# Optimization experiments

Hardware: AMD Instinct MI355X
Metric: run time of the kernel (lower is better)

The kernel has to match this reference:

```python
import jax, jax.numpy as jnp
import numpy as np

N_USER = 50000
N_ITEM = 50000
DIM = 128
HID = DIM // 2
E = 500000
SLOPE = 0.2  # GATv2 negative_slope default


def _glorot(key, shape):
    fan_in = shape[0]
    return jax.random.normal(key, shape, dtype=jnp.float32) / np.sqrt(fan_in)


def setup_inputs() -> dict:
    key = jax.random.key(0)
    ks = jax.random.split(key, 32)
    inp = {
        "x_user": jax.random.normal(ks[0], (N_USER, DIM), dtype=jnp.float32),
        "x_item": jax.random.normal(ks[1], (N_ITEM, DIM), dtype=jnp.float32),
        # edge[0] = source indices, edge[1] = destination indices
        "edge_u2i": jnp.stack([
            jax.random.randint(ks[2], (E,), 0, N_USER),
            jax.random.randint(ks[3], (E,), 0, N_ITEM),
        ]),
        "edge_i2u": jnp.stack([
            jax.random.randint(ks[4], (E,), 0, N_ITEM),
            jax.random.randint(ks[5], (E,), 0, N_USER),
        ]),
    }
    # per-node-type projection MLP: Linear(dim, dim//2) -> ReLU -> Linear(dim//2, dim)
    i = 6
    for t in ("user", "item"):
        inp[f"W1_{t}"] = _glorot(ks[i], (DIM, HID)); i += 1
        inp[f"b1_{t}"] = jnp.zeros((HID,), jnp.float32)
        inp[f"W2_{t}"] = _glorot(ks[i], (HID, DIM)); i += 1
        inp[f"b2_{t}"] = jnp.zeros((DIM,), jnp.float32)
    # per-edge-type GATv2 params (heads=1): lin_l (src), lin_r (dst), att, out bias
    for r in ("u2i", "i2u"):
        inp[f"Wl_{r}"] = _glorot(ks[i], (DIM, DIM)); i += 1
        inp[f"bl_{r}"] = jnp.zeros((DIM,), jnp.float32)
        inp[f"Wr_{r}"] = _glorot(ks[i], (DIM, DIM)); i += 1
        inp[f"br_{r}"] = jnp.zeros((DIM,), jnp.float32)
        inp[f"att_{r}"] = _glorot(ks[i], (DIM,)); i += 1
        inp[f"bias_{r}"] = jnp.zeros((DIM,), jnp.float32)
    return inp


def _mlp(x, W1, b1, W2, b2):
    return jax.nn.relu(x @ W1 + b1) @ W2 + b2


def _gatv2(x_src, x_dst, edge, Wl, bl, Wr, br, att, bias, n_dst):
    src, dst = edge[0], edge[1]
    xl = x_src @ Wl + bl                                    # [Ns, D]
    xr = x_dst @ Wr + br                                    # [Nd, D]
    z = jax.nn.leaky_relu(xl[src] + xr[dst], SLOPE)         # [E, D] gather
    logit = z @ att                                          # [E]
    # per-destination softmax over incoming edges
    m = jax.ops.segment_max(logit, dst, num_segments=n_dst)
    e = jnp.exp(logit - m[dst])
    s = jax.ops.segment_sum(e, dst, num_segments=n_dst)
    alpha = e / (s[dst] + 1e-16)                             # [E]
    out = jax.ops.segment_sum(alpha[:, None] * xl[src], dst, num_segments=n_dst)
    return out + bias


def reference(x_user, x_item, edge_u2i, edge_i2u,
              W1_user, b1_user, W2_user, b2_user,
              W1_item, b1_item, W2_item, b2_item,
              Wl_u2i, bl_u2i, Wr_u2i, br_u2i, att_u2i, bias_u2i,
              Wl_i2u, bl_i2u, Wr_i2u, br_i2u, att_i2u, bias_i2u):
    hu = _mlp(x_user, W1_user, b1_user, W2_user, b2_user)
    hi = _mlp(x_item, W1_item, b1_item, W2_item, b2_item)
    # HeteroConv with aggr='sum'; each dst type receives from one relation here
    out_item = _gatv2(hu, hi, edge_u2i, Wl_u2i, bl_u2i, Wr_u2i, br_u2i, att_u2i, bias_u2i, N_ITEM)
    out_user = _gatv2(hi, hu, edge_i2u, Wl_i2u, bl_i2u, Wr_i2u, br_i2u, att_i2u, bias_i2u, N_USER)
    return jnp.stack([out_user, out_item])  # [2, N, D] (N_USER == N_ITEM)
```

## Files before the change

kernel.cpp:

```cpp
#include <hip/hip_runtime.h>
#include <hip/hip_bf16.h>
#include <math.h>

#define N_NODES 50000
#define DIM 128
#define HID 64
#define SLOPE 0.2f
#define CAP 64
#define TRASH (2 * N_NODES * CAP)

typedef __attribute__((ext_vector_type(8))) short bf16x8;
typedef __attribute__((ext_vector_type(4))) float f32x4;
typedef __fp16 h2 __attribute__((ext_vector_type(2)));

#define OW1 0
#define OW2 8192
#define OWL 16384
#define OWR 32768
#define BLOB 49152
#define PREPB 192

static __device__ __forceinline__ ushort f2bf(float f) {
    uint u = __float_as_uint(f);
    u += 0x7FFFu + ((u >> 16) & 1u);
    return (ushort)(u >> 16);
}

static __device__ __forceinline__ uint pkh(float a, float b) {
    h2 r = __builtin_amdgcn_cvt_pkrtz(a, b);
    return __builtin_bit_cast(uint, r);
}

static __device__ __forceinline__ void prep_one(
    const float* __restrict__ W1, const float* __restrict__ W2,
    const float* __restrict__ Wl, const float* __restrict__ Wr,
    ushort* __restrict__ blob, int idx)
{
    const float* W; int NN, nkt, rel;
    if (idx < OW2)      { W = W1; NN = 64;  nkt = 4; rel = idx; }
    else if (idx < OWL) { W = W2; NN = 128; nkt = 2; rel = idx - OW2; }
    else if (idx < OWR) { W = Wl; NN = 128; nkt = 4; rel = idx - OWL; }
    else                { W = Wr; NN = 128; nkt = 4; rel = idx - OWR; }
    int j = rel & 7, l = (rel >> 3) & 63, t = rel >> 9;
    int kt = t % nkt, n = t / nkt;
    int k   = kt * 32 + (l >> 4) * 8 + j;
    int col = n * 16 + (l & 15);
    blob[idx] = f2bf(W[k * NN + col]);
}

__global__ __launch_bounds__(256) void prep_weights(
    const float* __restrict__ W1u, const float* __restrict__ W2u,
    const float* __restrict__ Wlu, const float* __restrict__ Wru,
    ushort* __restrict__ blobU,
    const float* __restrict__ W1i, const float* __restrict__ W2i,
    const float* __restrict__ Wli, const float* __restrict__ Wri,
    ushort* __restrict__ blobI,
    int* __restrict__ counts2)
{
    const int bid = blockIdx.x;
    const int gtid = bid * 256 + threadIdx.x;
    if (gtid < 2 * N_NODES) counts2[gtid] = 0;
    if (bid < PREPB) {
        prep_one(W1u, W2u, Wlu, Wru, blobU, bid * 256 + threadIdx.x);
    } else if (bid < 2 * PREPB) {
        prep_one(W1i, W2i, Wli, Wri, blobI, (bid - PREPB) * 256 + threadIdx.x);
    }
}

__global__ __launch_bounds__(512, 4) void k2_node_fill(
    const float* __restrict__ xA, const ushort* __restrict__ blobA,
    const float* __restrict__ b1A, const float* __restrict__ b2A,
    const float* __restrict__ blA, const float* __restrict__ brA,
    ushort* __restrict__ XLA, ushort* __restrict__ XRA,
    const float* __restrict__ xB, const ushort* __restrict__ blobB,
    const float* __restrict__ b1B, const float* __restrict__ b2B,
    const float* __restrict__ blB, const float* __restrict__ brB,
    ushort* __restrict__ XLB, ushort* __restrict__ XRB,
    int gnt, int M,
    const int* __restrict__ e1, int E1, const int* __restrict__ e2, int E2,
    int* __restrict__ counts2, ushort* __restrict__ slots16, int fillCount)
{
    __shared__ ushort hstage_all[8 * 16 * 136];
    const int tid = threadIdx.x;

    int bid = blockIdx.x;
    const int four = fillCount * 4;
    int wid; bool isfill;
    if (bid < four) {
        if ((bid & 3) == 3) { isfill = true;  wid = bid >> 2; }
        else                { isfill = false; wid = (bid >> 2) * 3 + (bid & 3); }
    } else { isfill = false; wid = 3 * fillCount + (bid - four); }

    if (isfill) {
        const int t = wid * 512 + tid;
        const int n1 = (E1 + 15) >> 4;
        const int n2 = (E2 + 15) >> 4;
        const int *sp, *dp; int base, E, off;
        if (t < n1)           { sp = e1; dp = e1 + E1; base = t * 16;        E = E1; off = 0; }
        else if (t < n1 + n2) { sp = e2; dp = e2 + E2; base = (t - n1) * 16; E = E2; off = N_NODES; }
        else return;
        if (base + 16 <= E) {
            int4 sv[4], dv[4];
            #pragma unroll
            for (int q = 0; q < 4; ++q) {
                sv[q] = *(const int4*)&sp[base + q * 4];
                dv[q] = *(const int4*)&dp[base + q * 4];
            }
            #pragma unroll
            for (int q = 0; q < 4; ++q) {
                int di, pos, addr;
                di = off + dv[q].x; pos = atomicAdd(&counts2[di], 1);
                addr = (pos < CAP) ? di * CAP + pos : TRASH;
                slots16[addr] = (ushort)sv[q].x;
                di = off + dv[q].y; pos = atomicAdd(&counts2[di], 1);
                addr = (pos < CAP) ? di * CAP + pos : TRASH;
                slots16[addr] = (ushort)sv[q].y;
                di = off + dv[q].z; pos = atomicAdd(&counts2[di], 1);
                addr = (pos < CAP) ? di * CAP + pos : TRASH;
                slots16[addr] = (ushort)sv[q].z;
                di = off + dv[q].w; pos = atomicAdd(&counts2[di], 1);
                addr = (pos < CAP) ? di * CAP + pos : TRASH;
                slots16[addr] = (ushort)sv[q].w;
            }
        } else {
            int hi = min(E, base + 16);
            for (int k = base; k < hi; ++k) {
                int di = off + dp[k];
                int pos = atomicAdd(&counts2[di], 1);
                int addr = (pos < CAP) ? di * CAP + pos : TRASH;
                slots16[addr] = (ushort)sp[k];
            }
        }
        return;
    }

    if (wid >= 2 * gnt) return;
    const float *x, *b1, *b2, *bl, *br;
    const ushort* blob;
    ushort *XL, *XR;
    int nbid = wid;
    if (nbid < gnt) {
        x = xA; blob = blobA; b1 = b1A; b2 = b2A; bl = blA; br = brA;
        XL = XLA; XR = XRA;
    } else {
        nbid -= gnt;
        x = xB; blob = blobB; b1 = b1B; b2 = b2B; bl = blB; br = brB;
        XL = XLB; XR = XRB;
    }

    const int wave = tid >> 6, lane = tid & 63;
    const int quad = lane & 15, half = lane >> 4;
    ushort* hstage = hstage_all + wave * (16 * 136);
    const int rbase = nbid * 256 + wave * 32;
    const int srow0 = min(rbase + quad,      M - 1);
    const int srow1 = min(rbase + 16 + quad, M - 1);

    bf16x8 a1[2][4];
    #pragma unroll
    for (int rt = 0; rt < 2; ++rt) {
        const int sr = rt ? srow1 : srow0;
        #pragma unroll
        for (int kt = 0; kt < 4; ++kt) {
            const float* p = &x[(size_t)sr * DIM + kt * 32 + half * 8];
            float4 f0 = *(const float4*)p;
            float4 f1 = *(const float4*)(p + 4);
            bf16x8 a;
            a[0] = (short)f2bf(f0.x); a[1] = (short)f2bf(f0.y);
            a[2] = (short)f2bf(f0.z); a[3] = (short)f2bf(f0.w);
            a[4] = (short)f2bf(f1.x); a[5] = (short)f2bf(f1.y);
            a[6] = (short)f2bf(f1.z); a[7] = (short)f2bf(f1.w);
            a1[rt][kt] = a;
        }
    }

    f32x4 hacc[2][4] = {};
    #pragma unroll
    for (int kt = 0; kt < 4; ++kt)
        #pragma unroll
        for (int n = 0; n < 4; ++n) {
            bf16x8 b = *(const bf16x8*)&blob[OW1 + (size_t)((n * 4 + kt) * 64 + lane) * 8];
            hacc[0][n] = __builtin_amdgcn_mfma_f32_16x16x32_bf16(b, a1[0][kt], hacc[0][n], 0, 0, 0);
            hacc[1][n] = __builtin_amdgcn_mfma_f32_16x16x32_bf16(b, a1[1][kt], hacc[1][n], 0, 0, 0);
        }

    bf16x8 a2[2][2];
    #pragma unroll
    for (int rt = 0; rt < 2; ++rt) {
        #pragma unroll
        for (int n = 0; n < 4; ++n) {
            const int col = n * 16 + half * 4;
            float4 bv = *(const float4*)&b1[col];
            ushort4 us;
            us.x = f2bf(fmaxf(hacc[rt][n][0] + bv.x, 0.f));
            us.y = f2bf(fmaxf(hacc[rt][n][1] + bv.y, 0.f));
            us.z = f2bf(fmaxf(hacc[rt][n][2] + bv.z, 0.f));
            us.w = f2bf(fmaxf(hacc[rt][n][3] + bv.w, 0.f));
            *(ushort4*)&hstage[quad * 136 + col] = us;
        }
        #pragma unroll
        for (int kt = 0; kt < 2; ++kt)
            a2[rt][kt] = *(const bf16x8*)&hstage[quad * 136 + kt * 32 + half * 8];
    }

    f32x4 h2acc[2][8] = {};
    #pragma unroll
    for (int kt = 0; kt < 2; ++kt)
        #pragma unroll
        for (int n = 0; n < 8; ++n) {
            bf16x8 b = *(const bf16x8*)&blob[OW2 + (size_t)((n * 2 + kt) * 64 + lane) * 8];
            h2acc[0][n] = __builtin_amdgcn_mfma_f32_16x16x32_bf16(b, a2[0][kt], h2acc[0][n], 0, 0, 0);
            h2acc[1][n] = __builtin_amdgcn_mfma_f32_16x16x32_bf16(b, a2[1][kt], h2acc[1][n], 0, 0, 0);
        }

    bf16x8 a3[2][4];
    #pragma unroll
    for (int rt = 0; rt < 2; ++rt) {
        #pragma unroll
        for (int n = 0; n < 8; ++n) {
            const int col = n * 16 + half * 4;
            float4 bv = *(const float4*)&b2[col];
            ushort4 us;
            us.x = f2bf(h2acc[rt][n][0] + bv.x);
            us.y = f2bf(h2acc[rt][n][1] + bv.y);
            us.z = f2bf(h2acc[rt][n][2] + bv.z);
            us.w = f2bf(h2acc[rt][n][3] + bv.w);
            *(ushort4*)&hstage[quad * 136 + col] = us;
        }
        #pragma unroll
        for (int kt = 0; kt < 4; ++kt)
            a3[rt][kt] = *(const bf16x8*)&hstage[quad * 136 + kt * 32 + half * 8];
    }

    const int r0 = rbase + quad;
    const int r1 = rbase + 16 + quad;
    #pragma unroll
    for (int n = 0; n < 8; ++n) {
        f32x4 aL0 = {}, aL1 = {}, aR0 = {}, aR1 = {};
        #pragma unroll
        for (int kt = 0; kt < 4; ++kt) {
            bf16x8 bL = *(const bf16x8*)&blob[OWL + (size_t)((n * 4 + kt) * 64 + lane) * 8];
            aL0 = __builtin_amdgcn_mfma_f32_16x16x32_bf16(bL, a3[0][kt], aL0, 0, 0, 0);
            aL1 = __builtin_amdgcn_mfma_f32_16x16x32_bf16(bL, a3[1][kt], aL1, 0, 0, 0);
            bf16x8 bR = *(const bf16x8*)&blob[OWR + (size_t)((n * 4 + kt) * 64 + lane) * 8];
            aR0 = __builtin_amdgcn_mfma_f32_16x16x32_bf16(bR, a3[0][kt], aR0, 0, 0, 0);
            aR1 = __builtin_amdgcn_mfma_f32_16x16x32_bf16(bR, a3[1][kt], aR1, 0, 0, 0);
        }
        const int col = n * 16 + half * 4;
        const float4 blv = *(const float4*)&bl[col];
        const float4 brv = *(const float4*)&br[col];
        if (r0 < M) {
            uint2 ul, ur;
            ul.x = pkh(aL0[0] + blv.x, aL0[1] + blv.y);
            ul.y = pkh(aL0[2] + blv.z, aL0[3] + blv.w);
            ur.x = pkh(aR0[0] + brv.x, aR0[1] + brv.y);
            ur.y = pkh(aR0[2] + brv.z, aR0[3] + brv.w);
            *(uint2*)&XL[(size_t)r0 * DIM + col] = ul;
            *(uint2*)&XR[(size_t)r0 * DIM + col] = ur;
        }
        if (r1 < M) {
            uint2 ul, ur;
            ul.x = pkh(aL1[0] + blv.x, aL1[1] + blv.y);
            ul.y = pkh(aL1[2] + blv.z, aL1[3] + blv.w);
            ur.x = pkh(aR1[0] + brv.x, aR1[1] + brv.y);
            ur.y = pkh(aR1[2] + brv.z, aR1[3] + brv.w);
            *(uint2*)&XL[(size_t)r1 * DIM + col] = ul;
            *(uint2*)&XR[(size_t)r1 * DIM + col] = ur;
        }
    }
}

static __device__ __forceinline__ float edge_logit_h(
    const h2* a, const h2* xrh, const float* at8, const h2 hs)
{
    float p = 0.f;
    #pragma unroll
    for (int pr = 0; pr < 4; ++pr) {
        h2 z  = a[pr] + xrh[pr];
        h2 zs = z * hs;
        h2 zl = __builtin_elementwise_max(z, zs);
        p = fmaf((float)zl[0], at8[2 * pr],     p);
        p = fmaf((float)zl[1], at8[2 * pr + 1], p);
    }
    return p;
}

__global__ __launch_bounds__(256) void gat_both(
    const ushort* __restrict__ xlA, const ushort* __restrict__ xrA,
    const float* __restrict__ attA, const float* __restrict__ biasA,
    float* __restrict__ outA,
    const ushort* __restrict__ xlB, const ushort* __restrict__ xrB,
    const float* __restrict__ attB, const float* __restrict__ biasB,
    float* __restrict__ outB,
    const int* __restrict__ counts2, const ushort* __restrict__ slots16)
{
    const int g    = (blockIdx.x * blockDim.x + threadIdx.x) >> 4;
    const int lane = threadIdx.x & 15;
    if (g >= 2 * N_NODES) return;

    const ushort *xl, *xr; const float *att, *bias; float* out; int gl;
    if (g < N_NODES) { xl = xlA; xr = xrA; att = attA; bias = biasA; out = outA; gl = g; }
    else { xl = xlB; xr = xrB; att = attB; bias = biasB; out = outB; gl = g - N_NODES; }

    const h2 hs = { (__fp16)SLOPE, (__fp16)SLOPE };
    h2 xrh[4];
    {
        uint4 u = *(const uint4*)&xr[(size_t)gl * DIM + lane * 8];
        xrh[0] = __builtin_bit_cast(h2, u.x);
        xrh[1] = __builtin_bit_cast(h2, u.y);
        xrh[2] = __builtin_bit_cast(h2, u.z);
        xrh[3] = __builtin_bit_cast(h2, u.w);
    }
    float at8[8];
    *(float4*)&at8[0] = *(const float4*)&att[lane * 8];
    *(float4*)&at8[4] = *(const float4*)&att[lane * 8 + 4];

    const int start = g * CAP;
    int deg = counts2[g];
    if (deg > CAP) deg = CAP;

    float m = -INFINITY, s = 0.f;
    float acc[8] = {};

    int i = 0;
    for (; i + 2 <= deg; i += 2) {
        int s0 = slots16[start + i];
        int s1 = slots16[start + i + 1];
        h2 a0[4], a1[4];
        {
            uint4 u = *(const uint4*)&xl[(size_t)s0 * DIM + lane * 8];
            a0[0] = __builtin_bit_cast(h2, u.x); a0[1] = __builtin_bit_cast(h2, u.y);
            a0[2] = __builtin_bit_cast(h2, u.z); a0[3] = __builtin_bit_cast(h2, u.w);
        }
        {
            uint4 u = *(const uint4*)&xl[(size_t)s1 * DIM + lane * 8];
            a1[0] = __builtin_bit_cast(h2, u.x); a1[1] = __builtin_bit_cast(h2, u.y);
            a1[2] = __builtin_bit_cast(h2, u.z); a1[3] = __builtin_bit_cast(h2, u.w);
        }
        float p0 = edge_logit_h(a0, xrh, at8, hs);
        float p1 = edge_logit_h(a1, xrh, at8, hs);
        #pragma unroll
        for (int o = 8; o; o >>= 1) {
            p0 += __shfl_xor(p0, o, 16);
            p1 += __shfl_xor(p1, o, 16);
        }
        float mn = fmaxf(p0, p1);
        if (mn > m + 8.f) {
            float sc = __expf(m - mn);
            s *= sc;
            #pragma unroll
            for (int d = 0; d < 8; ++d) acc[d] *= sc;
            m = mn;
        }
        float w0 = __expf(p0 - m);
        float w1 = __expf(p1 - m);
        s += w0 + w1;
        #pragma unroll
        for (int pr = 0; pr < 4; ++pr) {
            acc[2*pr]   = fmaf((float)a0[pr][0], w0, acc[2*pr]);
            acc[2*pr+1] = fmaf((float)a0[pr][1], w0, acc[2*pr+1]);
            acc[2*pr]   = fmaf((float)a1[pr][0], w1, acc[2*pr]);
            acc[2*pr+1] = fmaf((float)a1[pr][1], w1, acc[2*pr+1]);
        }
    }
    if (i < deg) {
        int s0 = slots16[start + i];
        h2 a0[4];
        {
            uint4 u = *(const uint4*)&xl[(size_t)s0 * DIM + lane * 8];
            a0[0] = __builtin_bit_cast(h2, u.x); a0[1] = __builtin_bit_cast(h2, u.y);
            a0[2] = __builtin_bit_cast(h2, u.z); a0[3] = __builtin_bit_cast(h2, u.w);
        }
        float p0 = edge_logit_h(a0, xrh, at8, hs);
        #pragma unroll
        for (int o = 8; o; o >>= 1) p0 += __shfl_xor(p0, o, 16);
        if (p0 > m + 8.f) {
            float sc = __expf(m - p0);
            s *= sc;
            #pragma unroll
            for (int d = 0; d < 8; ++d) acc[d] *= sc;
            m = p0;
        }
        float w0 = __expf(p0 - m);
        s += w0;
        #pragma unroll
        for (int pr = 0; pr < 4; ++pr) {
            acc[2*pr]   = fmaf((float)a0[pr][0], w0, acc[2*pr]);
            acc[2*pr+1] = fmaf((float)a0[pr][1], w0, acc[2*pr+1]);
        }
    }

    const float inv = 1.f / (s + 1e-16f);
    float o8[8];
    *(float4*)&o8[0] = *(const float4*)&bias[lane * 8];
    *(float4*)&o8[4] = *(const float4*)&bias[lane * 8 + 4];
    #pragma unroll
    for (int d = 0; d < 8; ++d) o8[d] = fmaf(acc[d], inv, o8[d]);
    float* op = &out[(size_t)gl * DIM + lane * 8];
    *(float4*)op       = *(const float4*)&o8[0];
    *(float4*)(op + 4) = *(const float4*)&o8[4];
}

extern "C" void kernel_launch(void* const* d_in, const int* in_sizes, int n_in,
                              void* d_out, int out_size, void* d_ws, size_t ws_size,
                              hipStream_t stream)
{
    const float* x_user   = (const float*)d_in[0];
    const float* x_item   = (const float*)d_in[1];
    const int*   edge_u2i = (const int*)d_in[2];
    const int*   edge_i2u = (const int*)d_in[3];
    const float* W1_user  = (const float*)d_in[4];
    const float* b1_user  = (const float*)d_in[5];
    const float* W2_user  = (const float*)d_in[6];
    const float* b2_user  = (const float*)d_in[7];
    const float* W1_item  = (const float*)d_in[8];
    const float* b1_item  = (const float*)d_in[9];
    const float* W2_item  = (const float*)d_in[10];
    const float* b2_item  = (const float*)d_in[11];
    const float* Wl_u2i   = (const float*)d_in[12];
    const float* bl_u2i   = (const float*)d_in[13];
    const float* Wr_u2i   = (const float*)d_in[14];
    const float* br_u2i   = (const float*)d_in[15];
    const float* att_u2i  = (const float*)d_in[16];
    const float* bias_u2i = (const float*)d_in[17];
    const float* Wl_i2u   = (const float*)d_in[18];
    const float* bl_i2u   = (const float*)d_in[19];
    const float* Wr_i2u   = (const float*)d_in[20];
    const float* br_i2u   = (const float*)d_in[21];
    const float* att_i2u  = (const float*)d_in[22];
    const float* bias_i2u = (const float*)d_in[23];

    const int E1 = in_sizes[2] / 2;
    const int E2 = in_sizes[3] / 2;

    const size_t NF = (size_t)N_NODES * DIM;
    ushort* XLu = (ushort*)d_ws;
    ushort* XRu = XLu + NF;
    ushort* XLi = XRu + NF;
    ushort* XRi = XLi + NF;
    ushort* blobU = XRi + NF;
    ushort* blobI = blobU + BLOB;
    int*    counts2 = (int*)(blobI + BLOB);
    ushort* slots16 = (ushort*)(counts2 + 2 * N_NODES);

    float* out_user = (float*)d_out;
    float* out_item = out_user + NF;

    dim3 blk(256);

    const int prepGrid = (2 * N_NODES + 255) / 256;
    prep_weights<<<(prepGrid > 2 * PREPB ? prepGrid : 2 * PREPB), blk, 0, stream>>>(
        W1_user, W2_user, Wl_u2i, Wr_i2u, blobU,
        W1_item, W2_item, Wl_i2u, Wr_u2i, blobI,
        counts2);

    const int nthr16 = ((E1 + 15) / 16) + ((E2 + 15) / 16);
    const int gnt = (N_NODES + 255) / 256;
    const int nodeCount = 2 * gnt;
    const int fillCount = (nthr16 + 511) / 512;
    const int totalB = nodeCount + fillCount;
    k2_node_fill<<<totalB, dim3(512), 0, stream>>>(
        x_user, blobU, b1_user, b2_user, bl_u2i, br_i2u, XLu, XRu,
        x_item, blobI, b1_item, b2_item, bl_i2u, br_u2i, XLi, XRi,
        gnt, N_NODES,
        edge_u2i, E1, edge_i2u, E2, counts2, slots16, fillCount);

    const int ng = (2 * N_NODES * 16 + 255) / 256;
    gat_both<<<ng, blk, 0, stream>>>(XLu, XRi, att_u2i, bias_u2i, out_item,
                                     XLi, XRu, att_i2u, bias_i2u, out_user,
                                     counts2, slots16);
}
```

Before: 130.6 us.

## Partition edge fill by destination residue and launch fill blocks after node blocks

The edge-bucketing fill stage is split into 8 passes. Each pass re-reads the same edge chunk but only handles destinations whose index mod 8 matches the pass, which is meant to cut atomic contention and scatter spread on the counts and slots arrays. The fill blocks are no longer interleaved with node-projection blocks; they now come after all node blocks in the grid. This reads the edge indices 8 times and launches 8x more fill blocks, and it loses the overlap the interleaving gave between fill and GEMM work.

After: 135.9 us. 1.04x slower.

```diff
diff --git a/kernel.cpp b/kernel.cpp
--- a/kernel.cpp
+++ b/kernel.cpp
@@ -78,21 +78,17 @@
     ushort* __restrict__ XLB, ushort* __restrict__ XRB,
     int gnt, int M,
     const int* __restrict__ e1, int E1, const int* __restrict__ e2, int E2,
-    int* __restrict__ counts2, ushort* __restrict__ slots16, int fillCount)
+    int* __restrict__ counts2, ushort* __restrict__ slots16, int nodeCount)
 {
     __shared__ ushort hstage_all[8 * 16 * 136];
     const int tid = threadIdx.x;
-
     int bid = blockIdx.x;
-    const int four = fillCount * 4;
-    int wid; bool isfill;
-    if (bid < four) {
-        if ((bid & 3) == 3) { isfill = true;  wid = bid >> 2; }
-        else                { isfill = false; wid = (bid >> 2) * 3 + (bid & 3); }
-    } else { isfill = false; wid = 3 * fillCount + (bid - four); }
-
-    if (isfill) {
-        const int t = wid * 512 + tid;
+
+    if (bid >= nodeCount) {
+        const int fb    = bid - nodeCount;
+        const int p     = fb & 7;
+        const int chunk = fb >> 3;
+        const int t = chunk * 512 + tid;
         const int n1 = (E1 + 15) >> 4;
         const int n2 = (E2 + 15) >> 4;
         const int *sp, *dp; int base, E, off;
@@ -108,37 +104,51 @@
             }
             #pragma unroll
             for (int q = 0; q < 4; ++q) {
-                int di, pos, addr;
-                di = off + dv[q].x; pos = atomicAdd(&counts2[di], 1);
-                addr = (pos < CAP) ? di * CAP + pos : TRASH;
-                slots16[addr] = (ushort)sv[q].x;
-                di = off + dv[q].y; pos = atomicAdd(&counts2[di], 1);
-                addr = (pos < CAP) ? di * CAP + pos : TRASH;
-                slots16[addr] = (ushort)sv[q].y;
-                di = off + dv[q].z; pos = atomicAdd(&counts2[di], 1);
-                addr = (pos < CAP) ? di * CAP + pos : TRASH;
-                slots16[addr] = (ushort)sv[q].z;
-                di = off + dv[q].w; pos = atomicAdd(&counts2[di], 1);
-                addr = (pos < CAP) ? di * CAP + pos : TRASH;
-                slots16[addr] = (ushort)sv[q].w;
+                int d, pos, addr;
+                d = dv[q].x;
+                if ((d & 7) == p) {
+                    int di = off + d; pos = atomicAdd(&counts2[di], 1);
+                    addr = (pos < CAP) ? di * CAP + pos : TRASH;
+                    slots16[addr] = (ushort)sv[q].x;
+                }
+                d = dv[q].y;
+                if ((d & 7) == p) {
+                    int di = off + d; pos = atomicAdd(&counts2[di], 1);
+                    addr = (pos < CAP) ? di * CAP + pos : TRASH;
+                    slots16[addr] = (ushort)sv[q].y;
+                }
+                d = dv[q].z;
+                if ((d & 7) == p) {
+                    int di = off + d; pos = atomicAdd(&counts2[di], 1);
+                    addr = (pos < CAP) ? di * CAP + pos : TRASH;
+                    slots16[addr] = (ushort)sv[q].z;
+                }
+                d = dv[q].w;
+                if ((d & 7) == p) {
+                    int di = off + d; pos = atomicAdd(&counts2[di], 1);
+                    addr = (pos < CAP) ? di * CAP + pos : TRASH;
+                    slots16[addr] = (ushort)sv[q].w;
+                }
             }
         } else {
             int hi = min(E, base + 16);
             for (int k = base; k < hi; ++k) {
-                int di = off + dp[k];
-                int pos = atomicAdd(&counts2[di], 1);
-                int addr = (pos < CAP) ? di * CAP + pos : TRASH;
-                slots16[addr] = (ushort)sp[k];
+                int d = dp[k];
+                if ((d & 7) == p) {
+                    int di = off + d;
+                    int pos = atomicAdd(&counts2[di], 1);
+                    int addr = (pos < CAP) ? di * CAP + pos : TRASH;
+                    slots16[addr] = (ushort)sp[k];
+                }
             }
         }
         return;
     }
 
-    if (wid >= 2 * gnt) return;
     const float *x, *b1, *b2, *bl, *br;
     const ushort* blob;
     ushort *XL, *XR;
-    int nbid = wid;
+    int nbid = bid;
     if (nbid < gnt) {
         x = xA; blob = blobA; b1 = b1A; b2 = b2A; bl = blA; br = brA;
         XL = XLA; XR = XRA;
@@ -456,13 +466,14 @@
     const int nthr16 = ((E1 + 15) / 16) + ((E2 + 15) / 16);
     const int gnt = (N_NODES + 255) / 256;
     const int nodeCount = 2 * gnt;
-    const int fillCount = (nthr16 + 511) / 512;
+    const int nchunks = (nthr16 + 511) / 512;
+    const int fillCount = nchunks * 8;
     const int totalB = nodeCount + fillCount;
     k2_node_fill<<<totalB, dim3(512), 0, stream>>>(
         x_user, blobU, b1_user, b2_user, bl_u2i, br_i2u, XLu, XRu,
         x_item, blobI, b1_item, b2_item, bl_i2u, br_u2i, XLi, XRi,
         gnt, N_NODES,
-        edge_u2i, E1, edge_i2u, E2, counts2, slots16, fillCount);
+        edge_u2i, E1, edge_i2u, E2, counts2, slots16, nodeCount);
 
     const int ng = (2 * N_NODES * 16 + 255) / 256;
     gat_both<<<ng, blk, 0, stream>>>(XLu, XRi, att_u2i, bias_u2i, out_item,
```
